# Optimization experiments

Hardware: AMD Instinct MI355X
Metric: run time of the kernel (lower is better)

Reference implementation:

```python
import jax, jax.numpy as jnp
import numpy as np

HID, H, KV, D = 2048, 16, 4, 128
B, L = 8, 1024
T = B * L
EPS = 1e-6
NEG = -1e9


def _rms(x, w):
    # RMSNorm over head_dim in fp32
    var = jnp.mean(x.astype(jnp.float32) ** 2, axis=-1, keepdims=True)
    return (x.astype(jnp.float32) * jax.lax.rsqrt(var + EPS)).astype(x.dtype) * w


def _rot_half(x):
    x1, x2 = jnp.split(x, 2, axis=-1)
    return jnp.concatenate([-x2, x1], axis=-1)


def setup_inputs() -> dict:
    key = jax.random.key(0)
    ks = jax.random.split(key, 24)
    inp = {}
    inp['packed_sequence'] = jax.random.normal(ks[0], (T, HID), jnp.float32) * 0.02
    # RoPE tables: positions restart per sample
    pos = jnp.tile(jnp.arange(L, dtype=jnp.float32), B)  # [T]
    inv_freq = 1.0 / (10000.0 ** (jnp.arange(0, D, 2, dtype=jnp.float32) / D))
    ang = pos[:, None] * inv_freq[None, :]  # [T, D/2]
    inp['cos'] = jnp.concatenate([jnp.cos(ang), jnp.cos(ang)], axis=-1)
    inp['sin'] = jnp.concatenate([jnp.sin(ang), jnp.sin(ang)], axis=-1)
    # per-sample causal additive mask [B, L, L]
    causal = jnp.tril(jnp.ones((L, L), bool))
    inp['attn_bias'] = jnp.broadcast_to(jnp.where(causal, 0.0, NEG).astype(jnp.float32), (B, L, L))
    inp['gen_mask'] = jax.random.randint(ks[1], (T,), 0, 2, jnp.int32)
    s = 0.02
    inp['Wq'] = jax.random.normal(ks[2], (H * D, HID), jnp.float32) * s
    inp['bq'] = jnp.zeros((H * D,), jnp.float32)
    inp['Wqg'] = jax.random.normal(ks[3], (H * D, HID), jnp.float32) * s
    inp['bqg'] = jnp.zeros((H * D,), jnp.float32)
    inp['Wk'] = jax.random.normal(ks[4], (KV * D, HID), jnp.float32) * s
    inp['bk'] = jnp.zeros((KV * D,), jnp.float32)
    inp['Wkg'] = jax.random.normal(ks[5], (KV * D, HID), jnp.float32) * s
    inp['bkg'] = jnp.zeros((KV * D,), jnp.float32)
    inp['Wv'] = jax.random.normal(ks[6], (KV * D, HID), jnp.float32) * s
    inp['bv'] = jnp.zeros((KV * D,), jnp.float32)
    inp['Wvg'] = jax.random.normal(ks[7], (KV * D, HID), jnp.float32) * s
    inp['bvg'] = jnp.zeros((KV * D,), jnp.float32)
    inp['Wo'] = jax.random.normal(ks[8], (HID, H * D), jnp.float32) * s
    inp['Wog'] = jax.random.normal(ks[9], (HID, H * D), jnp.float32) * s
    inp['q_norm_w'] = jnp.ones((D,), jnp.float32)
    inp['q_norm_gen_w'] = jnp.ones((D,), jnp.float32)
    inp['k_norm_w'] = jnp.ones((D,), jnp.float32)
    inp['k_norm_gen_w'] = jnp.ones((D,), jnp.float32)
    return inp


def reference(packed_sequence, cos, sin, attn_bias, gen_mask,
              Wq, bq, Wqg, bqg, Wk, bk, Wkg, bkg, Wv, bv, Wvg, bvg,
              Wo, Wog, q_norm_w, q_norm_gen_w, k_norm_w, k_norm_gen_w):
    route = (gen_mask > 0)[:, None]  # [T,1]; und/gen indexes partition tokens -> select
    # dual-path QKV projections (scatter into zero buffers == per-token select)
    q = jnp.where(route, packed_sequence @ Wqg.T + bqg, packed_sequence @ Wq.T + bq)
    k = jnp.where(route, packed_sequence @ Wkg.T + bkg, packed_sequence @ Wk.T + bk)
    v = jnp.where(route, packed_sequence @ Wvg.T + bvg, packed_sequence @ Wv.T + bv)
    q = q.reshape(T, H, D)
    k = k.reshape(T, KV, D)
    v = v.reshape(T, KV, D)
    rh = route[:, :, None]  # [T,1,1]
    # dual-path per-head-dim RMSNorm
    q = jnp.where(rh, _rms(q, q_norm_gen_w), _rms(q, q_norm_w))
    k = jnp.where(rh, _rms(k, k_norm_gen_w), _rms(k, k_norm_w))
    # RoPE (broadcast over heads, unsqueeze_dim=1)
    c, s = cos[:, None, :], sin[:, None, :]
    q = q * c + _rot_half(q) * s
    k = k * c + _rot_half(k) * s
    # GQA: repeat kv heads to H
    k = jnp.repeat(k, H // KV, axis=1)
    v = jnp.repeat(v, H // KV, axis=1)
    # ragged attention, equal sample lens -> batched SDPA with per-sample masks
    qb = q.reshape(B, L, H, D)
    kb = k.reshape(B, L, H, D)
    vb = v.reshape(B, L, H, D)
    scores = jnp.einsum('blhd,bmhd->bhlm', qb, kb) / np.sqrt(D).astype(np.float32)
    scores = scores + attn_bias[:, None, :, :]
    p = jax.nn.softmax(scores, axis=-1)
    o = jnp.einsum('bhlm,bmhd->blhd', p, vb).reshape(T, H * D)
    # dual-path output projection (no bias)
    return jnp.where(route, o @ Wog.T, o @ Wo.T)
```

## Files before the change

kernel.cpp:

```cpp
#include <hip/hip_runtime.h>

#define T_TOK 8192
#define HID   2048
#define NH    16
#define NKV   4
#define HD    128

typedef __attribute__((ext_vector_type(8))) short short8;
typedef __attribute__((ext_vector_type(4))) float f32x4;
typedef __attribute__((ext_vector_type(4))) unsigned short us4;

__device__ __forceinline__ unsigned short f2b(float f) {
  union { float f; unsigned int u; } x; x.f = f;
  unsigned int u = x.u;
  return (unsigned short)((u + 0x7FFFu + ((u >> 16) & 1u)) >> 16);
}
__device__ __forceinline__ float b2f(unsigned short u) {
  union { float f; unsigned int u; } x; x.u = ((unsigned int)u) << 16; return x.f;
}

__device__ __forceinline__ void ld_lds16(const unsigned short* g, unsigned short* l) {
  __builtin_amdgcn_global_load_lds(
      (const __attribute__((address_space(1))) unsigned int*)g,
      (__attribute__((address_space(3))) unsigned int*)l, 16, 0, 0);
}

__global__ __launch_bounds__(1024) void scan_route(const int* __restrict__ gm,
                                                   int* __restrict__ perm,
                                                   int* __restrict__ n0p) {
  __shared__ int cnt[1024];
  int tid = threadIdx.x;
  int base = tid * 8;
  int r[8]; int c0 = 0;
#pragma unroll
  for (int i = 0; i < 8; i++) { r[i] = gm[base + i] > 0 ? 1 : 0; c0 += 1 - r[i]; }
  cnt[tid] = c0;
  __syncthreads();
  for (int off = 1; off < 1024; off <<= 1) {
    int add = (tid >= off) ? cnt[tid - off] : 0;
    __syncthreads();
    cnt[tid] += add;
    __syncthreads();
  }
  int incl = cnt[tid];
  int total0 = cnt[1023];
  int p0 = incl - c0;
  int p1 = total0 + (base - (incl - c0));
#pragma unroll
  for (int i = 0; i < 8; i++) {
    int t = base + i;
    if (r[i] == 0) perm[p0++] = t;
    else           perm[p1++] = t;
  }
  if (tid == 0) n0p[0] = total0;
}

struct ConvArgs {
  const float* src[9];
  unsigned short* dst[9];
  int blk_end[9];
};

__global__ __launch_bounds__(256) void convert_all(ConvArgs a) {
  int blk = blockIdx.x;
  int s = 0;
  while (blk >= a.blk_end[s]) s++;
  int local = blk - (s ? a.blk_end[s - 1] : 0);
  int i = local * 1024 + threadIdx.x * 4;
  float4 v = *(const float4*)(a.src[s] + i);
  us4 o = { f2b(v.x), f2b(v.y), f2b(v.z), f2b(v.w) };
  *(us4*)(a.dst[s] + i) = o;
}

#define BM  128
#define BK  64

__device__ __forceinline__ void gemm_core(
    const unsigned short* __restrict__ Xb,
    const unsigned short* __restrict__ W,
    const float* __restrict__ bias,
    const int* __restrict__ perm,
    int r0, int r1, int col0, int N,
    float* __restrict__ outF, unsigned short* __restrict__ outB,
    unsigned short* As, unsigned short* Bs)
{
  int tid = threadIdx.x;
  int lane = tid & 63, wid = tid >> 6;
  int quad = lane >> 4, l15 = lane & 15;
  int wr = (wid >> 1) * 64, wc = (wid & 1) * 64;
  int lrow = lane >> 3;
  int sc8 = (lane & 7) ^ (lrow & 7);

  const unsigned short* ag[4]; const unsigned short* bg[4];
  unsigned short* al[4]; unsigned short* bl[4];
#pragma unroll
  for (int i = 0; i < 4; i++) {
    int row = wid * 32 + i * 8 + lrow;
    int gr = r0 + row; if (gr > r1 - 1) gr = r1 - 1;
    ag[i] = Xb + (size_t)perm[gr] * HID + sc8 * 8;
    bg[i] = W + (size_t)(col0 + row) * HID + sc8 * 8;
    al[i] = As + (wid * 32 + i * 8) * BK;
    bl[i] = Bs + (wid * 32 + i * 8) * BK;
  }

  f32x4 zero = {0.f, 0.f, 0.f, 0.f};
  f32x4 acc[4][4];
#pragma unroll
  for (int a = 0; a < 4; a++)
#pragma unroll
    for (int b = 0; b < 4; b++) acc[a][b] = zero;

  for (int k0 = 0; k0 < HID; k0 += BK) {
#pragma unroll
    for (int i = 0; i < 4; i++) {
      ld_lds16(ag[i] + k0, al[i]);
      ld_lds16(bg[i] + k0, bl[i]);
    }
    __syncthreads();
#pragma unroll
    for (int kk = 0; kk < 2; kk++) {
      int cswz = ((kk * 4 + quad) ^ (l15 & 7)) * 8;
      short8 af[4], bf[4];
#pragma unroll
      for (int mt = 0; mt < 4; mt++)
        af[mt] = *(const short8*)&As[(wr + mt * 16 + l15) * BK + cswz];
#pragma unroll
      for (int nt = 0; nt < 4; nt++)
        bf[nt] = *(const short8*)&Bs[(wc + nt * 16 + l15) * BK + cswz];
#pragma unroll
      for (int mt = 0; mt < 4; mt++)
#pragma unroll
        for (int nt = 0; nt < 4; nt++)
          acc[mt][nt] = __builtin_amdgcn_mfma_f32_16x16x32_bf16(af[mt], bf[nt], acc[mt][nt], 0, 0, 0);
    }
    __syncthreads();
  }

#pragma unroll
  for (int mt = 0; mt < 4; mt++) {
#pragma unroll
    for (int r = 0; r < 4; r++) {
      int lr = wr + mt * 16 + quad * 4 + r;
      int gr = r0 + lr;
      if (gr >= r1) continue;
      int tok = perm[gr];
#pragma unroll
      for (int nt = 0; nt < 4; nt++) {
        int col = col0 + wc + nt * 16 + l15;
        float v = acc[mt][nt][r];
        if (bias) v += bias[col];
        if (outF) outF[(size_t)tok * N + col] = v;
        else      outB[(size_t)tok * N + col] = f2b(v);
      }
    }
  }
}

__global__ __launch_bounds__(256, 3) void gemm_qkv(
    const unsigned short* __restrict__ xb,
    const unsigned short* wq0, const unsigned short* wq1,
    const float* bq0, const float* bq1,
    const unsigned short* wk0, const unsigned short* wk1,
    const float* bk0, const float* bk1,
    const unsigned short* wv0, const unsigned short* wv1,
    const float* bv0, const float* bv1,
    unsigned short* qraw, unsigned short* kraw, unsigned short* vb,
    const int* __restrict__ perm, const int* __restrict__ n0p)
{
  __shared__ unsigned short As[BM * BK];
  __shared__ unsigned short Bs[BM * BK];
  int set = blockIdx.z;
  int n0 = n0p[0];
  int r0, r1;
  if (set == 0) { r0 = blockIdx.x * BM; if (r0 >= n0) return; r1 = (r0 + BM < n0) ? r0 + BM : n0; }
  else          { r0 = n0 + blockIdx.x * BM; if (r0 >= T_TOK) return; r1 = (r0 + BM < T_TOK) ? r0 + BM : T_TOK; }
  int y = blockIdx.y;
  const unsigned short* w; const float* bias;
  unsigned short* ob; int col0, N;
  if (y < 16)      { w = set ? wq1 : wq0; bias = set ? bq1 : bq0; col0 = y * 128;        N = HID; ob = qraw; }
  else if (y < 20) { w = set ? wk1 : wk0; bias = set ? bk1 : bk0; col0 = (y - 16) * 128; N = 512; ob = kraw; }
  else             { w = set ? wv1 : wv0; bias = set ? bv1 : bv0; col0 = (y - 20) * 128; N = 512; ob = vb; }
  gemm_core(xb, w, bias, perm, r0, r1, col0, N, nullptr, ob, As, Bs);
}

__global__ __launch_bounds__(256, 3) void gemm_out(
    const unsigned short* __restrict__ obuf,
    const unsigned short* wo0, const unsigned short* wo1,
    float* __restrict__ out,
    const int* __restrict__ perm, const int* __restrict__ n0p)
{
  __shared__ unsigned short As[BM * BK];
  __shared__ unsigned short Bs[BM * BK];
  int set = blockIdx.z;
  int n0 = n0p[0];
  int r0, r1;
  if (set == 0) { r0 = blockIdx.x * BM; if (r0 >= n0) return; r1 = (r0 + BM < n0) ? r0 + BM : n0; }
  else          { r0 = n0 + blockIdx.x * BM; if (r0 >= T_TOK) return; r1 = (r0 + BM < T_TOK) ? r0 + BM : T_TOK; }
  gemm_core(obuf, set ? wo1 : wo0, nullptr, perm, r0, r1, blockIdx.y * 128, HID, out, nullptr, As, Bs);
}

__global__ __launch_bounds__(256) void rms_rope(
    const unsigned short* __restrict__ in, unsigned short* __restrict__ outp,
    const float* __restrict__ cosb, const float* __restrict__ sinb,
    const int* __restrict__ gm,
    const float* __restrict__ wn, const float* __restrict__ wg, int nh)
{
  int wvid = blockIdx.x * 4 + (threadIdx.x >> 6);
  int lane = threadIdx.x & 63;
  int t = wvid / nh, h = wvid - t * nh;
  size_t off = ((size_t)t * nh + h) * HD;
  float x1 = b2f(in[off + lane]), x2 = b2f(in[off + 64 + lane]);
  float ss = x1 * x1 + x2 * x2;
#pragma unroll
  for (int o = 32; o > 0; o >>= 1) ss += __shfl_xor(ss, o, 64);
  float inv = rsqrtf(ss * (1.0f / 128.0f) + 1e-6f);
  const float* w = (gm[t] > 0) ? wg : wn;
  float n1 = x1 * inv * w[lane];
  float n2 = x2 * inv * w[lane + 64];
  float c1 = cosb[t * HD + lane],      s1 = sinb[t * HD + lane];
  float c2 = cosb[t * HD + 64 + lane], s2 = sinb[t * HD + 64 + lane];
  outp[off + lane]      = f2b(n1 * c1 - n2 * s1);
  outp[off + 64 + lane] = f2b(n2 * c2 + n1 * s2);
}

__global__ __launch_bounds__(256) void vtrans(const unsigned short* __restrict__ vb,
                                              unsigned short* __restrict__ vt) {
  __shared__ unsigned short Vs[64][136];
  int kt = blockIdx.x, kvh = blockIdx.y, b = blockIdx.z;
  int t = threadIdx.x;
  int kv0 = kt * 64;
  int key = t >> 2, c0 = t & 3;
#pragma unroll
  for (int i = 0; i < 4; i++) {
    int cc = c0 * 4 + i;
    *(short8*)&Vs[key][cc * 8] =
        *(const short8*)(vb + ((size_t)(b * 1024 + kv0 + key) * NKV + kvh) * HD + cc * 8);
  }
  __syncthreads();
  int d = t >> 1, hh = t & 1;
  unsigned short tmp[32];
#pragma unroll
  for (int k = 0; k < 32; k++) tmp[k] = Vs[hh * 32 + k][d];
  size_t base = ((size_t)(b * NKV + kvh) * HD + d) * 1024 + kv0 + hh * 32;
  *(short8*)(vt + base)      = *(short8*)&tmp[0];
  *(short8*)(vt + base + 8)  = *(short8*)&tmp[8];
  *(short8*)(vt + base + 16) = *(short8*)&tmp[16];
  *(short8*)(vt + base + 24) = *(short8*)&tmp[24];
}

__global__ __launch_bounds__(512, 2) void attn_kernel(
    const unsigned short* __restrict__ qb,
    const unsigned short* __restrict__ kb,
    const unsigned short* __restrict__ vt,
    unsigned short* __restrict__ ob)
{
  __shared__ unsigned short Ks[64 * 128];
  __shared__ unsigned short Vt[128 * 64];
  __shared__ unsigned short Ps[8 * 16 * 64];
  int pslot = blockIdx.x, kvh = blockIdx.y, b = blockIdx.z;
  int tid = threadIdx.x, lane = tid & 63, wid = tid >> 6;
  int quad = lane >> 4, l15 = lane & 15;
  int h = kvh * 4 + (wid >> 1);
  int g = wid & 1;
  const float sc = 0.088388347648318447f;
  f32x4 zero = {0.f, 0.f, 0.f, 0.f};

  int skey = (wid << 2) + (lane >> 4);
  int kswz = ((lane & 15) ^ (skey & 7)) * 8;
  int sd   = (wid << 3) + (lane >> 3);
  int vswz = ((lane & 7) ^ (sd & 7)) * 8;

  for (int half = 0; half < 2; half++) {
    int a = half ? (31 - pslot) : pslot;
    int q0 = a * 32;
    int qrow = q0 + g * 16 + l15;
    size_t qoff = ((size_t)(b * 1024 + qrow) * NH + h) * HD;
    short8 qfr[4];
#pragma unroll
    for (int kk = 0; kk < 4; kk++)
      qfr[kk] = *(const short8*)(qb + qoff + kk * 32 + quad * 8);

    f32x4 oacc[8];
#pragma unroll
    for (int i = 0; i < 8; i++) oacc[i] = zero;
    float lpart[4] = {0.f, 0.f, 0.f, 0.f};

    int ktiles = a / 2 + 1;
    for (int kt = 0; kt < ktiles; kt++) {
      int kv0 = kt * 64;
      __syncthreads();
#pragma unroll
      for (int i = 0; i < 2; i++) {
        int key = i * 32 + skey;
        ld_lds16(kb + ((size_t)(b * 1024 + kv0 + key) * NKV + kvh) * HD + kswz,
                 Ks + (size_t)(i * 32 + (wid << 2)) * 128);
      }
#pragma unroll
      for (int i = 0; i < 2; i++) {
        int d = i * 64 + sd;
        ld_lds16(vt + ((size_t)(b * NKV + kvh) * HD + d) * 1024 + kv0 + vswz,
                 Vt + (size_t)(i * 64 + (wid << 3)) * 64);
      }
      __syncthreads();
      bool lastt = (kt == ktiles - 1);

      f32x4 s[4];
#pragma unroll
      for (int g4 = 0; g4 < 4; g4++) {
        f32x4 acc = zero;
#pragma unroll
        for (int kk = 0; kk < 4; kk++) {
          short8 bfr = *(const short8*)&Ks[(g4 * 16 + l15) * 128 + ((kk * 4 + quad) ^ (l15 & 7)) * 8];
          acc = __builtin_amdgcn_mfma_f32_16x16x32_bf16(qfr[kk], bfr, acc, 0, 0, 0);
        }
        s[g4] = acc;
      }
      int rowb = q0 + g * 16 + quad * 4;
#pragma unroll
      for (int g4 = 0; g4 < 4; g4++) {
        int col = kv0 + g4 * 16 + l15;
        int k8 = g4 * 2 + (l15 >> 3);
#pragma unroll
        for (int r = 0; r < 4; r++) {
          float p = __expf(s[g4][r] * sc);
          if (lastt && col > rowb + r) p = 0.f;
          lpart[r] += p;
          int row = quad * 4 + r;
          Ps[wid * 1024 + row * 64 + ((k8 ^ (row & 7)) * 8 + (l15 & 7))] = f2b(p);
        }
      }
#pragma unroll
      for (int kk = 0; kk < 2; kk++) {
        short8 pa = *(const short8*)&Ps[wid * 1024 + l15 * 64 + ((kk * 4 + quad) ^ (l15 & 7)) * 8];
#pragma unroll
        for (int dg = 0; dg < 8; dg++) {
          short8 vf = *(const short8*)&Vt[(dg * 16 + l15) * 64 + ((kk * 4 + quad) ^ (l15 & 7)) * 8];
          oacc[dg] = __builtin_amdgcn_mfma_f32_16x16x32_bf16(pa, vf, oacc[dg], 0, 0, 0);
        }
      }
    }
#pragma unroll
    for (int r = 0; r < 4; r++) {
      float v = lpart[r];
#pragma unroll
      for (int o = 8; o > 0; o >>= 1) v += __shfl_xor(v, o, 64);
      lpart[r] = 1.0f / v;
    }
#pragma unroll
    for (int dg = 0; dg < 8; dg++)
#pragma unroll
      for (int r = 0; r < 4; r++) {
        int row = q0 + g * 16 + quad * 4 + r;
        ob[((size_t)(b * 1024 + row) * NH + h) * HD + dg * 16 + l15] =
            f2b(oacc[dg][r] * lpart[r]);
      }
  }
}

extern "C" void kernel_launch(void* const* d_in, const int* in_sizes, int n_in,
                              void* d_out, int out_size, void* d_ws, size_t ws_size,
                              hipStream_t stream) {
  const float* x    = (const float*)d_in[0];
  const float* cosb = (const float*)d_in[1];
  const float* sinb = (const float*)d_in[2];
  const int*   gm   = (const int*)d_in[4];
  const float* Wq   = (const float*)d_in[5];
  const float* bq   = (const float*)d_in[6];
  const float* Wqg  = (const float*)d_in[7];
  const float* bqg  = (const float*)d_in[8];
  const float* Wk   = (const float*)d_in[9];
  const float* bk   = (const float*)d_in[10];
  const float* Wkg  = (const float*)d_in[11];
  const float* bkg  = (const float*)d_in[12];
  const float* Wv   = (const float*)d_in[13];
  const float* bv   = (const float*)d_in[14];
  const float* Wvg  = (const float*)d_in[15];
  const float* bvg  = (const float*)d_in[16];
  const float* Wo   = (const float*)d_in[17];
  const float* Wog  = (const float*)d_in[18];
  const float* qnw  = (const float*)d_in[19];
  const float* qngw = (const float*)d_in[20];
  const float* knw  = (const float*)d_in[21];
  const float* kngw = (const float*)d_in[22];
  float* out = (float*)d_out;

  char* wsb = (char*)d_ws;
  size_t off = 0;
  auto alloc = [&](size_t bytes) -> char* {
    char* p = wsb + off;
    off += (bytes + 255) & ~(size_t)255;
    return p;
  };
  int* perm = (int*)alloc((size_t)T_TOK * 4);
  int* n0p  = (int*)alloc(4);
  unsigned short* xb  = (unsigned short*)alloc((size_t)T_TOK * HID * 2);
  unsigned short* wq0 = (unsigned short*)alloc((size_t)HID * HID * 2);
  unsigned short* wq1 = (unsigned short*)alloc((size_t)HID * HID * 2);
  unsigned short* wk0 = (unsigned short*)alloc((size_t)512 * HID * 2);
  unsigned short* wk1 = (unsigned short*)alloc((size_t)512 * HID * 2);
  unsigned short* wv0 = (unsigned short*)alloc((size_t)512 * HID * 2);
  unsigned short* wv1 = (unsigned short*)alloc((size_t)512 * HID * 2);
  unsigned short* wo0 = (unsigned short*)alloc((size_t)HID * HID * 2);
  unsigned short* wo1 = (unsigned short*)alloc((size_t)HID * HID * 2);
  unsigned short* qraw = (unsigned short*)alloc((size_t)T_TOK * HID * 2);
  unsigned short* kraw = (unsigned short*)alloc((size_t)T_TOK * 512 * 2);
  unsigned short* vbuf = (unsigned short*)alloc((size_t)T_TOK * 512 * 2);
  unsigned short* vtb  = (unsigned short*)alloc((size_t)T_TOK * 512 * 2);
  unsigned short* qbuf = (unsigned short*)alloc((size_t)T_TOK * HID * 2);
  unsigned short* kbuf = (unsigned short*)alloc((size_t)T_TOK * 512 * 2);
  unsigned short* obuf = qraw;

  scan_route<<<dim3(1), dim3(1024), 0, stream>>>(gm, perm, n0p);

  ConvArgs ca;
  const float* srcs[9] = {x, Wq, Wqg, Wk, Wkg, Wv, Wvg, Wo, Wog};
  unsigned short* dsts[9] = {xb, wq0, wq1, wk0, wk1, wv0, wv1, wo0, wo1};
  int ns[9] = {T_TOK * HID, HID * HID, HID * HID, 512 * HID, 512 * HID,
               512 * HID, 512 * HID, HID * HID, HID * HID};
  int cum = 0;
  for (int i = 0; i < 9; i++) {
    ca.src[i] = srcs[i]; ca.dst[i] = dsts[i];
    cum += ns[i] / 1024; ca.blk_end[i] = cum;
  }
  convert_all<<<dim3(cum), dim3(256), 0, stream>>>(ca);

  gemm_qkv<<<dim3(64, 24, 2), dim3(256), 0, stream>>>(
      xb, wq0, wq1, bq, bqg, wk0, wk1, bk, bkg, wv0, wv1, bv, bvg,
      qraw, kraw, vbuf, perm, n0p);

  rms_rope<<<dim3(T_TOK * NH / 4), dim3(256), 0, stream>>>(
      qraw, qbuf, cosb, sinb, gm, qnw, qngw, NH);
  rms_rope<<<dim3(T_TOK * NKV / 4), dim3(256), 0, stream>>>(
      kraw, kbuf, cosb, sinb, gm, knw, kngw, NKV);
  vtrans<<<dim3(16, 4, 8), dim3(256), 0, stream>>>(vbuf, vtb);

  attn_kernel<<<dim3(16, 4, 8), dim3(512), 0, stream>>>(qbuf, kbuf, vtb, obuf);

  gemm_out<<<dim3(64, 16, 2), dim3(256), 0, stream>>>(obuf, wo0, wo1, out, perm, n0p);
}
```

Baseline: 591.7 us.

## Pre-permute activations by route, fuse rms_rope launches, widen attention per-wave rows

The activation conversion now writes x directly into route-sorted order via an inverse permutation, so the QKV and output GEMMs load contiguous A rows instead of gathering through perm. Q/K stay in sorted order out of the GEMM and a single fused rms_rope kernel scatters them back to token order. V is still scattered in the GEMM epilogue. Attention output is written in sorted order for gemm_out. Attention now uses 4 waves per block, each handling two 16-row query groups, which reuses K/V fragments across both groups but raises register pressure.

```diff
diff --git a/kernel.cpp b/kernel.cpp
--- a/kernel.cpp
+++ b/kernel.cpp
@@ -27,6 +27,7 @@
 
 __global__ __launch_bounds__(1024) void scan_route(const int* __restrict__ gm,
                                                    int* __restrict__ perm,
+                                                   int* __restrict__ invperm,
                                                    int* __restrict__ n0p) {
   __shared__ int cnt[1024];
   int tid = threadIdx.x;
@@ -49,8 +50,8 @@
 #pragma unroll
   for (int i = 0; i < 8; i++) {
     int t = base + i;
-    if (r[i] == 0) perm[p0++] = t;
-    else           perm[p1++] = t;
+    if (r[i] == 0) { perm[p0] = t; invperm[t] = p0; p0++; }
+    else           { perm[p1] = t; invperm[t] = p1; p1++; }
   }
   if (tid == 0) n0p[0] = total0;
 }
@@ -61,7 +62,7 @@
   int blk_end[9];
 };
 
-__global__ __launch_bounds__(256) void convert_all(ConvArgs a) {
+__global__ __launch_bounds__(256) void convert_all(ConvArgs a, const int* __restrict__ invperm) {
   int blk = blockIdx.x;
   int s = 0;
   while (blk >= a.blk_end[s]) s++;
@@ -69,7 +70,12 @@
   int i = local * 1024 + threadIdx.x * 4;
   float4 v = *(const float4*)(a.src[s] + i);
   us4 o = { f2b(v.x), f2b(v.y), f2b(v.z), f2b(v.w) };
-  *(us4*)(a.dst[s] + i) = o;
+  if (s == 0) {
+    int row = i >> 11, col = i & 2047;
+    *(us4*)(a.dst[0] + (size_t)invperm[row] * 2048 + col) = o;
+  } else {
+    *(us4*)(a.dst[s] + i) = o;
+  }
 }
 
 #define BM  128
@@ -79,7 +85,7 @@
     const unsigned short* __restrict__ Xb,
     const unsigned short* __restrict__ W,
     const float* __restrict__ bias,
-    const int* __restrict__ perm,
+    const int* __restrict__ permEpi,
     int r0, int r1, int col0, int N,
     float* __restrict__ outF, unsigned short* __restrict__ outB,
     unsigned short* As, unsigned short* Bs)
@@ -96,8 +102,7 @@
 #pragma unroll
   for (int i = 0; i < 4; i++) {
     int row = wid * 32 + i * 8 + lrow;
-    int gr = r0 + row; if (gr > r1 - 1) gr = r1 - 1;
-    ag[i] = Xb + (size_t)perm[gr] * HID + sc8 * 8;
+    ag[i] = Xb + (size_t)(r0 + row) * HID + sc8 * 8;
     bg[i] = W + (size_t)(col0 + row) * HID + sc8 * 8;
     al[i] = As + (wid * 32 + i * 8) * BK;
     bl[i] = Bs + (wid * 32 + i * 8) * BK;
@@ -143,7 +148,7 @@
       int lr = wr + mt * 16 + quad * 4 + r;
       int gr = r0 + lr;
       if (gr >= r1) continue;
-      int tok = perm[gr];
+      int tok = permEpi ? permEpi[gr] : gr;
 #pragma unroll
       for (int nt = 0; nt < 4; nt++) {
         int col = col0 + wc + nt * 16 + l15;
@@ -176,11 +181,11 @@
   else          { r0 = n0 + blockIdx.x * BM; if (r0 >= T_TOK) return; r1 = (r0 + BM < T_TOK) ? r0 + BM : T_TOK; }
   int y = blockIdx.y;
   const unsigned short* w; const float* bias;
-  unsigned short* ob; int col0, N;
-  if (y < 16)      { w = set ? wq1 : wq0; bias = set ? bq1 : bq0; col0 = y * 128;        N = HID; ob = qraw; }
-  else if (y < 20) { w = set ? wk1 : wk0; bias = set ? bk1 : bk0; col0 = (y - 16) * 128; N = 512; ob = kraw; }
-  else             { w = set ? wv1 : wv0; bias = set ? bv1 : bv0; col0 = (y - 20) * 128; N = 512; ob = vb; }
-  gemm_core(xb, w, bias, perm, r0, r1, col0, N, nullptr, ob, As, Bs);
+  unsigned short* ob; int col0, N; const int* pe;
+  if (y < 16)      { w = set ? wq1 : wq0; bias = set ? bq1 : bq0; col0 = y * 128;        N = HID; ob = qraw; pe = nullptr; }
+  else if (y < 20) { w = set ? wk1 : wk0; bias = set ? bk1 : bk0; col0 = (y - 16) * 128; N = 512; ob = kraw; pe = nullptr; }
+  else             { w = set ? wv1 : wv0; bias = set ? bv1 : bv0; col0 = (y - 20) * 128; N = 512; ob = vb;   pe = perm; }
+  gemm_core(xb, w, bias, pe, r0, r1, col0, N, nullptr, ob, As, Bs);
 }
 
 __global__ __launch_bounds__(256, 3) void gemm_out(
@@ -199,17 +204,34 @@
   gemm_core(obuf, set ? wo1 : wo0, nullptr, perm, r0, r1, blockIdx.y * 128, HID, out, nullptr, As, Bs);
 }
 
-__global__ __launch_bounds__(256) void rms_rope(
-    const unsigned short* __restrict__ in, unsigned short* __restrict__ outp,
+__global__ __launch_bounds__(256) void rms_rope_all(
+    const unsigned short* __restrict__ qraw, const unsigned short* __restrict__ kraw,
+    unsigned short* __restrict__ qbuf, unsigned short* __restrict__ kbuf,
     const float* __restrict__ cosb, const float* __restrict__ sinb,
-    const int* __restrict__ gm,
-    const float* __restrict__ wn, const float* __restrict__ wg, int nh)
+    const int* __restrict__ perm, const int* __restrict__ gm,
+    const float* __restrict__ qnw, const float* __restrict__ qngw,
+    const float* __restrict__ knw, const float* __restrict__ kngw)
 {
   int wvid = blockIdx.x * 4 + (threadIdx.x >> 6);
   int lane = threadIdx.x & 63;
-  int t = wvid / nh, h = wvid - t * nh;
-  size_t off = ((size_t)t * nh + h) * HD;
-  float x1 = b2f(in[off + lane]), x2 = b2f(in[off + 64 + lane]);
+  const unsigned short* in; unsigned short* outp;
+  const float *wn, *wg;
+  int t;
+  if (wvid < T_TOK * NH) {
+    int r = wvid >> 4, h = wvid & 15;
+    t = perm[r];
+    in = qraw + ((size_t)r * NH + h) * HD;
+    outp = qbuf + ((size_t)t * NH + h) * HD;
+    wn = qnw; wg = qngw;
+  } else {
+    int w2 = wvid - T_TOK * NH;
+    int r = w2 >> 2, h = w2 & 3;
+    t = perm[r];
+    in = kraw + ((size_t)r * NKV + h) * HD;
+    outp = kbuf + ((size_t)t * NKV + h) * HD;
+    wn = knw; wg = kngw;
+  }
+  float x1 = b2f(in[lane]), x2 = b2f(in[64 + lane]);
   float ss = x1 * x1 + x2 * x2;
 #pragma unroll
   for (int o = 32; o > 0; o >>= 1) ss += __shfl_xor(ss, o, 64);
@@ -219,8 +241,8 @@
   float n2 = x2 * inv * w[lane + 64];
   float c1 = cosb[t * HD + lane],      s1 = sinb[t * HD + lane];
   float c2 = cosb[t * HD + 64 + lane], s2 = sinb[t * HD + 64 + lane];
-  outp[off + lane]      = f2b(n1 * c1 - n2 * s1);
-  outp[off + 64 + lane] = f2b(n2 * c2 + n1 * s2);
+  outp[lane]      = f2b(n1 * c1 - n2 * s1);
+  outp[64 + lane] = f2b(n2 * c2 + n1 * s2);
 }
 
 __global__ __launch_bounds__(256) void vtrans(const unsigned short* __restrict__ vb,
@@ -248,20 +270,20 @@
   *(short8*)(vt + base + 24) = *(short8*)&tmp[24];
 }
 
-__global__ __launch_bounds__(512, 2) void attn_kernel(
+__global__ __launch_bounds__(256, 2) void attn_kernel(
     const unsigned short* __restrict__ qb,
     const unsigned short* __restrict__ kb,
     const unsigned short* __restrict__ vt,
+    const int* __restrict__ invperm,
     unsigned short* __restrict__ ob)
 {
   __shared__ unsigned short Ks[64 * 128];
   __shared__ unsigned short Vt[128 * 64];
-  __shared__ unsigned short Ps[8 * 16 * 64];
+  __shared__ unsigned short Ps[4 * 32 * 64];
   int pslot = blockIdx.x, kvh = blockIdx.y, b = blockIdx.z;
   int tid = threadIdx.x, lane = tid & 63, wid = tid >> 6;
   int quad = lane >> 4, l15 = lane & 15;
-  int h = kvh * 4 + (wid >> 1);
-  int g = wid & 1;
+  int h = kvh * 4 + wid;
   const float sc = 0.088388347648318447f;
   f32x4 zero = {0.f, 0.f, 0.f, 0.f};
 
@@ -273,87 +295,102 @@
   for (int half = 0; half < 2; half++) {
     int a = half ? (31 - pslot) : pslot;
     int q0 = a * 32;
-    int qrow = q0 + g * 16 + l15;
-    size_t qoff = ((size_t)(b * 1024 + qrow) * NH + h) * HD;
-    short8 qfr[4];
-#pragma unroll
-    for (int kk = 0; kk < 4; kk++)
-      qfr[kk] = *(const short8*)(qb + qoff + kk * 32 + quad * 8);
-
-    f32x4 oacc[8];
-#pragma unroll
-    for (int i = 0; i < 8; i++) oacc[i] = zero;
-    float lpart[4] = {0.f, 0.f, 0.f, 0.f};
+    short8 qfr[2][4];
+#pragma unroll
+    for (int g = 0; g < 2; g++) {
+      size_t qoff = ((size_t)(b * 1024 + q0 + g * 16 + l15) * NH + h) * HD;
+#pragma unroll
+      for (int kk = 0; kk < 4; kk++)
+        qfr[g][kk] = *(const short8*)(qb + qoff + kk * 32 + quad * 8);
+    }
+    f32x4 oacc[2][8];
+#pragma unroll
+    for (int g = 0; g < 2; g++)
+#pragma unroll
+      for (int i = 0; i < 8; i++) oacc[g][i] = zero;
+    float lp[2][4] = {{0.f,0.f,0.f,0.f},{0.f,0.f,0.f,0.f}};
 
     int ktiles = a / 2 + 1;
     for (int kt = 0; kt < ktiles; kt++) {
       int kv0 = kt * 64;
       __syncthreads();
 #pragma unroll
-      for (int i = 0; i < 2; i++) {
-        int key = i * 32 + skey;
-        ld_lds16(kb + ((size_t)(b * 1024 + kv0 + key) * NKV + kvh) * HD + kswz,
-                 Ks + (size_t)(i * 32 + (wid << 2)) * 128);
-      }
-#pragma unroll
-      for (int i = 0; i < 2; i++) {
-        int d = i * 64 + sd;
-        ld_lds16(vt + ((size_t)(b * NKV + kvh) * HD + d) * 1024 + kv0 + vswz,
-                 Vt + (size_t)(i * 64 + (wid << 3)) * 64);
-      }
+      for (int i = 0; i < 4; i++)
+        ld_lds16(kb + ((size_t)(b * 1024 + kv0 + i * 16 + skey) * NKV + kvh) * HD + kswz,
+                 Ks + (size_t)(i * 16 + (wid << 2)) * 128);
+#pragma unroll
+      for (int i = 0; i < 4; i++)
+        ld_lds16(vt + ((size_t)(b * NKV + kvh) * HD + (i * 32 + sd)) * 1024 + kv0 + vswz,
+                 Vt + (size_t)(i * 32 + (wid << 3)) * 64);
       __syncthreads();
       bool lastt = (kt == ktiles - 1);
 
-      f32x4 s[4];
+      f32x4 s[2][4];
 #pragma unroll
       for (int g4 = 0; g4 < 4; g4++) {
-        f32x4 acc = zero;
-#pragma unroll
-        for (int kk = 0; kk < 4; kk++) {
-          short8 bfr = *(const short8*)&Ks[(g4 * 16 + l15) * 128 + ((kk * 4 + quad) ^ (l15 & 7)) * 8];
-          acc = __builtin_amdgcn_mfma_f32_16x16x32_bf16(qfr[kk], bfr, acc, 0, 0, 0);
+        short8 bfr[4];
+#pragma unroll
+        for (int kk = 0; kk < 4; kk++)
+          bfr[kk] = *(const short8*)&Ks[(g4 * 16 + l15) * 128 + ((kk * 4 + quad) ^ (l15 & 7)) * 8];
+#pragma unroll
+        for (int g = 0; g < 2; g++) {
+          f32x4 acc = zero;
+#pragma unroll
+          for (int kk = 0; kk < 4; kk++)
+            acc = __builtin_amdgcn_mfma_f32_16x16x32_bf16(qfr[g][kk], bfr[kk], acc, 0, 0, 0);
+          s[g][g4] = acc;
         }
-        s[g4] = acc;
-      }
-      int rowb = q0 + g * 16 + quad * 4;
-#pragma unroll
-      for (int g4 = 0; g4 < 4; g4++) {
-        int col = kv0 + g4 * 16 + l15;
-        int k8 = g4 * 2 + (l15 >> 3);
-#pragma unroll
-        for (int r = 0; r < 4; r++) {
-          float p = __expf(s[g4][r] * sc);
-          if (lastt && col > rowb + r) p = 0.f;
-          lpart[r] += p;
-          int row = quad * 4 + r;
-          Ps[wid * 1024 + row * 64 + ((k8 ^ (row & 7)) * 8 + (l15 & 7))] = f2b(p);
+      }
+#pragma unroll
+      for (int g = 0; g < 2; g++) {
+#pragma unroll
+        for (int g4 = 0; g4 < 4; g4++) {
+          int col = kv0 + g4 * 16 + l15;
+          int k8 = g4 * 2 + (l15 >> 3);
+#pragma unroll
+          for (int r = 0; r < 4; r++) {
+            float p = __expf(s[g][g4][r] * sc);
+            int row = q0 + g * 16 + quad * 4 + r;
+            if (lastt && col > row) p = 0.f;
+            lp[g][r] += p;
+            int rloc = g * 16 + quad * 4 + r;
+            Ps[wid * 2048 + rloc * 64 + ((k8 ^ (rloc & 7)) * 8 + (l15 & 7))] = f2b(p);
+          }
         }
       }
 #pragma unroll
       for (int kk = 0; kk < 2; kk++) {
-        short8 pa = *(const short8*)&Ps[wid * 1024 + l15 * 64 + ((kk * 4 + quad) ^ (l15 & 7)) * 8];
+        short8 pa[2];
+#pragma unroll
+        for (int g = 0; g < 2; g++)
+          pa[g] = *(const short8*)&Ps[wid * 2048 + (g * 16 + l15) * 64 + ((kk * 4 + quad) ^ (l15 & 7)) * 8];
 #pragma unroll
         for (int dg = 0; dg < 8; dg++) {
           short8 vf = *(const short8*)&Vt[(dg * 16 + l15) * 64 + ((kk * 4 + quad) ^ (l15 & 7)) * 8];
-          oacc[dg] = __builtin_amdgcn_mfma_f32_16x16x32_bf16(pa, vf, oacc[dg], 0, 0, 0);
+#pragma unroll
+          for (int g = 0; g < 2; g++)
+            oacc[g][dg] = __builtin_amdgcn_mfma_f32_16x16x32_bf16(pa[g], vf, oacc[g][dg], 0, 0, 0);
         }
       }
     }
 #pragma unroll
-    for (int r = 0; r < 4; r++) {
-      float v = lpart[r];
-#pragma unroll
-      for (int o = 8; o > 0; o >>= 1) v += __shfl_xor(v, o, 64);
-      lpart[r] = 1.0f / v;
-    }
-#pragma unroll
-    for (int dg = 0; dg < 8; dg++)
+    for (int g = 0; g < 2; g++) {
+#pragma unroll
+      for (int r = 0; r < 4; r++) {
+        float v = lp[g][r];
+#pragma unroll
+        for (int o = 8; o > 0; o >>= 1) v += __shfl_xor(v, o, 64);
+        lp[g][r] = 1.0f / v;
+      }
 #pragma unroll
       for (int r = 0; r < 4; r++) {
         int row = q0 + g * 16 + quad * 4 + r;
-        ob[((size_t)(b * 1024 + row) * NH + h) * HD + dg * 16 + l15] =
-            f2b(oacc[dg][r] * lpart[r]);
-      }
+        int prow = invperm[b * 1024 + row];
+#pragma unroll
+        for (int dg = 0; dg < 8; dg++)
+          ob[(size_t)prow * HID + h * 128 + dg * 16 + l15] = f2b(oacc[g][dg][r] * lp[g][r]);
+      }
+    }
   }
 }
 
@@ -391,8 +428,9 @@
     off += (bytes + 255) & ~(size_t)255;
     return p;
   };
-  int* perm = (int*)alloc((size_t)T_TOK * 4);
-  int* n0p  = (int*)alloc(4);
+  int* perm    = (int*)alloc((size_t)T_TOK * 4);
+  int* invperm = (int*)alloc((size_t)T_TOK * 4);
+  int* n0p     = (int*)alloc(4);
   unsigned short* xb  = (unsigned short*)alloc((size_t)T_TOK * HID * 2);
   unsigned short* wq0 = (unsigned short*)alloc((size_t)HID * HID * 2);
   unsigned short* wq1 = (unsigned short*)alloc((size_t)HID * HID * 2);
@@ -410,7 +448,7 @@
   unsigned short* kbuf = (unsigned short*)alloc((size_t)T_TOK * 512 * 2);
   unsigned short* obuf = qraw;
 
-  scan_route<<<dim3(1), dim3(1024), 0, stream>>>(gm, perm, n0p);
+  scan_route<<<dim3(1), dim3(1024), 0, stream>>>(gm, perm, invperm, n0p);
 
   ConvArgs ca;
   const float* srcs[9] = {x, Wq, Wqg, Wk, Wkg, Wv, Wvg, Wo, Wog};
@@ -422,19 +460,17 @@
     ca.src[i] = srcs[i]; ca.dst[i] = dsts[i];
     cum += ns[i] / 1024; ca.blk_end[i] = cum;
   }
-  convert_all<<<dim3(cum), dim3(256), 0, stream>>>(ca);
+  convert_all<<<dim3(cum), dim3(256), 0, stream>>>(ca, invperm);
 
   gemm_qkv<<<dim3(64, 24, 2), dim3(256), 0, stream>>>(
       xb, wq0, wq1, bq, bqg, wk0, wk1, bk, bkg, wv0, wv1, bv, bvg,
       qraw, kraw, vbuf, perm, n0p);
 
-  rms_rope<<<dim3(T_TOK * NH / 4), dim3(256), 0, stream>>>(
-      qraw, qbuf, cosb, sinb, gm, qnw, qngw, NH);
-  rms_rope<<<dim3(T_TOK * NKV / 4), dim3(256), 0, stream>>>(
-      kraw, kbuf, cosb, sinb, gm, knw, kngw, NKV);
+  rms_rope_all<<<dim3((T_TOK * (NH + NKV)) / 4), dim3(256), 0, stream>>>(
+      qraw, kraw, qbuf, kbuf, cosb, sinb, perm, gm, qnw, qngw, knw, kngw);
   vtrans<<<dim3(16, 4, 8), dim3(256), 0, stream>>>(vbuf, vtb);
 
-  attn_kernel<<<dim3(16, 4, 8), dim3(512), 0, stream>>>(qbuf, kbuf, vtb, obuf);
+  attn_kernel<<<dim3(16, 4, 8), dim3(256), 0, stream>>>(qbuf, kbuf, vtb, invperm, obuf);
 
   gemm_out<<<dim3(64, 16, 2), dim3(256), 0, stream>>>(obuf, wo0, wo1, out, perm, n0p);
 }
```

Measured after the change: 595.2 us. No clear change (+0.6%).
